# Optimization experiments

Hardware: AMD Instinct MI355X
Metric: run time of the kernel (lower is better)

## Reference

```python
import jax, jax.numpy as jnp
import numpy as np

BATCH = 8192
IN_FEATURES = 128
OUT_FEATURES = 256
GRID_SIZE = 20
ORDER = 3
L = GRID_SIZE + ORDER  # coeffs length per edge = 23


def setup_inputs() -> dict:
    key = jax.random.key(0)
    kx, kc = jax.random.split(key)
    x = jax.random.normal(kx, (BATCH, IN_FEATURES), dtype=jnp.float32)
    # fused per-edge B-spline coefficients: [out_features, in_features, grid_size+order]
    coeffs = jax.random.normal(kc, (OUT_FEATURES, IN_FEATURES, L), dtype=jnp.float32) * 0.1
    return {"x": x, "coeffs": coeffs}


def reference(x, coeffs):
    # x: [B, I], coeffs: [O, I, L]
    O, I, Lc = coeffs.shape
    B = x.shape[0]
    s = jax.nn.sigmoid(x)                      # x_clamped in (0, 1)
    idx = s * (GRID_SIZE - 1)                  # fractional bin index in [0, 19)
    k = idx.astype(jnp.int32)                  # trunc == floor since idx >= 0
    w1 = idx - k.astype(x.dtype)
    w0 = 1.0 - w1
    k0 = jnp.clip(k, 0, Lc - 1)                # [B, I]
    k1 = jnp.clip(k + 1, 0, Lc - 1)
    # Build sparse interpolation weights [B, I, L] (two nonzeros per (b, j)),
    # then contract against the shared coefficient tensor in one fused reduce:
    # out[b, i] = sum_j c[i, j, k0[b,j]] * w0[b,j] + c[i, j, k1[b,j]] * w1[b,j]
    brow = jnp.arange(B)[:, None]
    jcol = jnp.arange(I)[None, :]
    W = jnp.zeros((B, I, Lc), dtype=x.dtype)
    W = W.at[brow, jcol, k0].add(w0)
    W = W.at[brow, jcol, k1].add(w1)
    return jnp.einsum('bjl,ijl->bi', W, coeffs)  # [B, O]
```

## Files before the change

kernel.cpp:

```cpp
#include <hip/hip_runtime.h>
#include <hip/hip_fp16.h>

#define BATCH 8192
#define IN_F 128
#define OUT_F 256
#define LC 23
#define BROW 768
#define JPW 16

typedef _Float16 f16x8 __attribute__((ext_vector_type(8)));
typedef float f32x4 __attribute__((ext_vector_type(4)));
typedef _Float16 half2v __attribute__((ext_vector_type(2)));

__global__ __launch_bounds__(256) void prep_kernel(
    const float* __restrict__ coeffs, _Float16* __restrict__ cp2) {
    int t = blockIdx.x * 256 + threadIdx.x;
    int col = t & 15;
    int u = t >> 4;
    int q = u % 3;
    int v = u / 3;
    int g = v & 15;
    int j = v >> 4;
    int i = g * 16 + col;
    int s0 = q * 8;
    const float* src = coeffs + ((size_t)i * IN_F + j) * LC;
    f16x8 w;
#pragma unroll
    for (int e = 0; e < 8; ++e) {
        int s = s0 + e;
        float f = (s < 20) ? src[s] : 0.0f;
        w[e] = (_Float16)f;
    }
    char* dst = reinterpret_cast<char*>(cp2) +
                (size_t)(j * 16 + g) * BROW + q * 256 + col * 16;
    *reinterpret_cast<f16x8*>(dst) = w;
}

__global__ __launch_bounds__(512, 2) void kan_mfma7(
    const float* __restrict__ x, const char* __restrict__ cp2,
    float* __restrict__ out) {
    __shared__ uint2 mlds[IN_F][64];

    const int tid = threadIdx.x;
    const int lane = tid & 63;
    const int ks = tid >> 6;
    const int l15 = lane & 15;
    const int q = lane >> 4;
    const int q4 = q * 4;
    const int qc = (q < 3) ? q : 2;

    int wg = (blockIdx.x & 7) * 32 + (blockIdx.x >> 3);
    const int mb = wg >> 1;
    const int bn = wg & 1;
    const int b0 = mb * 64;

    {
        const int row = tid & 63;
        const int jb = (tid >> 6) * 16;
        const float4* xr = reinterpret_cast<const float4*>(
            x + (size_t)(b0 + row) * IN_F + jb);
#pragma unroll
        for (int u = 0; u < 4; ++u) {
            float4 xv = xr[u];
#pragma unroll
            for (int e = 0; e < 4; ++e) {
                float xvv = (e == 0) ? xv.x : (e == 1) ? xv.y
                           : (e == 2) ? xv.z : xv.w;
                float s = 1.0f / (1.0f + __expf(-xvv));
                float idxf = s * 19.0f;
                int k = (int)idxf;
                k = (k > 18) ? 18 : k;
                float w1 = idxf - (float)k;
                float w0 = 1.0f - w1;
                unsigned u0 = __half_as_ushort(__float2half(w0));
                unsigned u1 = __half_as_ushort(__float2half(w1));
                unsigned lo, hi;
                if (k & 1) { lo = u0 << 16; hi = u1; }
                else       { lo = u0 | (u1 << 16); hi = 0u; }
                unsigned P = (unsigned)(k >> 1);
                mlds[jb + u * 4 + e][row] = uint2{lo, hi | (P << 16)};
            }
        }
    }
    __syncthreads();

    const int j0 = ks * JPW;
    const char* bbase = cp2 + (size_t)(bn * 8) * BROW + qc * 256 + l15 * 16;
    auto bld = [&](int j, int nf) {
        return *reinterpret_cast<const f16x8*>(
            bbase + (size_t)(j * 16 + nf) * BROW);
    };

    f32x4 acc[4][8];
#pragma unroll
    for (int mf = 0; mf < 4; ++mf)
#pragma unroll
        for (int nf = 0; nf < 8; ++nf) acc[mf][nf] = f32x4{0.f, 0.f, 0.f, 0.f};

    f16x8 r1[4], r2[4];
#pragma unroll
    for (int h = 0; h < 4; ++h) r1[h] = bld(j0, h);

#pragma unroll 2
    for (int jj = 0; jj < JPW; ++jj) {
        const int j = j0 + jj;
#pragma unroll
        for (int h = 0; h < 4; ++h) r2[h] = bld(j, 4 + h);
        f16x8 au[4];
        {
            const uint2* mrow = &mlds[j][0];
#pragma unroll
            for (int mf = 0; mf < 4; ++mf) {
                uint2 m = mrow[mf * 16 + l15];
                unsigned lo = m.x;
                unsigned hi = m.y & 0xFFFFu;
                int d = (int)(m.y >> 16) - q4;
                union { uint32_t u[4]; f16x8 h; } a;
#pragma unroll
                for (int r = 0; r < 4; ++r) {
                    uint32_t v = (d == r) ? lo : 0u;
                    v = (d == r - 1) ? hi : v;
                    a.u[r] = v;
                }
                au[mf] = a.h;
            }
        }
#pragma unroll
        for (int mf = 0; mf < 4; ++mf)
#pragma unroll
            for (int nf = 0; nf < 4; ++nf)
                acc[mf][nf] = __builtin_amdgcn_mfma_f32_16x16x32_f16(
                    au[mf], r1[nf], acc[mf][nf], 0, 0, 0);
        if (jj + 1 < JPW) {
#pragma unroll
            for (int h = 0; h < 4; ++h) r1[h] = bld(j + 1, h);
        }
#pragma unroll
        for (int mf = 0; mf < 4; ++mf)
#pragma unroll
            for (int nf = 0; nf < 4; ++nf)
                acc[mf][4 + nf] = __builtin_amdgcn_mfma_f32_16x16x32_f16(
                    au[mf], r2[nf], acc[mf][4 + nf], 0, 0, 0);
    }

    __syncthreads();
    float* red = reinterpret_cast<float*>(&mlds[0][0]);
#pragma unroll
    for (int pass = 0; pass < 4; ++pass) {
#pragma unroll
        for (int mf = 0; mf < 4; ++mf)
#pragma unroll
            for (int t = 0; t < 2; ++t)
#pragma unroll
                for (int r = 0; r < 4; ++r)
                    red[ks * 2048 + (mf * 16 + q4 + r) * 32 + t * 16 + l15] =
                        acc[mf][pass * 2 + t][r];
        __syncthreads();
#pragma unroll
        for (int it = 0; it < 4; ++it) {
            int idx = it * 512 + tid;
            float s = 0.f;
#pragma unroll
            for (int w = 0; w < 8; ++w) s += red[w * 2048 + idx];
            int row = idx >> 5;
            int col = idx & 31;
            out[(size_t)(b0 + row) * OUT_F + bn * 128 + pass * 32 + col] = s;
        }
        __syncthreads();
    }
}

__device__ __forceinline__ float dot2_acc(unsigned cbits, unsigned wbits,
                                          float acc) {
#if __has_builtin(__builtin_amdgcn_fdot2)
    union { unsigned u; half2v h; } c, w;
    c.u = cbits; w.u = wbits;
    return __builtin_amdgcn_fdot2(c.h, w.h, acc, false);
#else
    __half2 hc = *reinterpret_cast<const __half2*>(&cbits);
    __half2 hw = *reinterpret_cast<const __half2*>(&wbits);
    float2 fc = __half22float2(hc);
    float2 fw = __half22float2(hw);
    return acc + fc.x * fw.x + fc.y * fw.y;
#endif
}

__global__ __launch_bounds__(256) void build_ctg_kernel(
    const float* __restrict__ coeffs, unsigned short* __restrict__ ctg) {
    int tid = blockIdx.x * 256 + threadIdx.x;
    int qq = tid & 63;
    int k = (tid >> 6) % LC;
    int j = tid / (64 * LC);
    if (j >= IN_F) return;
    int k1 = (k + 1 < LC) ? (k + 1) : (LC - 1);
    union { unsigned short h[8]; uint4 v; } u;
#pragma unroll
    for (int c = 0; c < 4; ++c) {
        int i = qq * 4 + c;
        const float* base = coeffs + ((size_t)i * IN_F + j) * LC;
        u.h[2 * c]     = __half_as_ushort(__float2half(base[k]));
        u.h[2 * c + 1] = __half_as_ushort(__float2half(base[k1]));
    }
    reinterpret_cast<uint4*>(ctg)[tid] = u.v;
}

__global__ __launch_bounds__(256) void kan_main_kernel(
    const float* __restrict__ x, const char* __restrict__ ctg,
    float* __restrict__ out) {
    __shared__ unsigned metas[4][2 * IN_F];
    const int wave = threadIdx.x >> 6;
    const int lane = threadIdx.x & 63;
    const int b = blockIdx.x * 4 + wave;
    float2 xv = reinterpret_cast<const float2*>(x + (size_t)b * IN_F)[lane];
    uint4 m;
#pragma unroll
    for (int t = 0; t < 2; ++t) {
        float xs = t ? xv.y : xv.x;
        float s = 1.0f / (1.0f + __expf(-xs));
        float idxf = s * 19.0f;
        int k = (int)idxf;
        k = (k > 18) ? 18 : k;
        float w1 = idxf - (float)k;
        float w0 = 1.0f - w1;
        int j = 2 * lane + t;
        unsigned off = (unsigned)((j * LC + k) << 10);
        half2v w; w[0] = (_Float16)w0; w[1] = (_Float16)w1;
        unsigned wbits = *reinterpret_cast<unsigned*>(&w);
        if (t == 0) { m.x = off; m.y = wbits; }
        else        { m.z = off; m.w = wbits; }
    }
    reinterpret_cast<uint4*>(&metas[wave][0])[lane] = m;
    __syncthreads();
    const unsigned lanebase = lane * 16;
    const uint4* mrow = reinterpret_cast<const uint4*>(&metas[wave][0]);
    float acc0 = 0.f, acc1 = 0.f, acc2 = 0.f, acc3 = 0.f;
#pragma unroll 8
    for (int j2 = 0; j2 < IN_F / 2; ++j2) {
        uint4 mm = mrow[j2];
        {
            const uint4 e = *reinterpret_cast<const uint4*>(
                ctg + (size_t)(lanebase + mm.x));
            acc0 = dot2_acc(e.x, mm.y, acc0);
            acc1 = dot2_acc(e.y, mm.y, acc1);
            acc2 = dot2_acc(e.z, mm.y, acc2);
            acc3 = dot2_acc(e.w, mm.y, acc3);
        }
        {
            const uint4 e = *reinterpret_cast<const uint4*>(
                ctg + (size_t)(lanebase + mm.z));
            acc0 = dot2_acc(e.x, mm.w, acc0);
            acc1 = dot2_acc(e.y, mm.w, acc1);
            acc2 = dot2_acc(e.z, mm.w, acc2);
            acc3 = dot2_acc(e.w, mm.w, acc3);
        }
    }
    float4 r = make_float4(acc0, acc1, acc2, acc3);
    reinterpret_cast<float4*>(out + (size_t)b * OUT_F)[lane] = r;
}

extern "C" void kernel_launch(void* const* d_in, const int* in_sizes, int n_in,
                              void* d_out, int out_size, void* d_ws,
                              size_t ws_size, hipStream_t stream) {
    const float* x = (const float*)d_in[0];
    const float* coeffs = (const float*)d_in[1];
    float* out = (float*)d_out;

    const size_t cp2_bytes = (size_t)IN_F * 16 * BROW;
    const size_t ctg_bytes = (size_t)IN_F * LC * 64 * 16;

    if (d_ws != nullptr && ws_size >= cp2_bytes) {
        _Float16* cp2 = (_Float16*)d_ws;
        prep_kernel<<<384, 256, 0, stream>>>(coeffs, cp2);
        kan_mfma7<<<256, 512, 0, stream>>>(x, (const char*)cp2, out);
    } else if (d_ws != nullptr && ws_size >= ctg_bytes) {
        char* ctg = (char*)d_ws;
        const int totalA = IN_F * LC * 64;
        build_ctg_kernel<<<(totalA + 255) / 256, 256, 0, stream>>>(
            coeffs, (unsigned short*)ctg);
        kan_main_kernel<<<BATCH / 4, 256, 0, stream>>>(x, ctg, out);
    } else {
        kan_main_kernel<<<BATCH / 4, 256, 0, stream>>>(x, (const char*)d_ws,
                                                       out);
    }
}
```

Baseline: 31.20 us.

## Halve output tile per block to double grid and raise occupancy

Each block now computes 64 output columns instead of 128, so the grid doubles to 512 blocks and launch bounds request 4 blocks per CU. The accumulator array and B-fragment registers halve, and the loop becomes a two-stage ping-pong prefetch of coefficient fragments. The reduction buffer writes use a swizzled column index to cut LDS bank conflicts, and one barrier is dropped. In exchange, the sigmoid/weight preprocessing of x is now repeated by twice as many blocks, and the LDS footprint (64 KB per block) may cap how many blocks actually reside per CU.

```diff
diff --git a/kernel.cpp b/kernel.cpp
--- a/kernel.cpp
+++ b/kernel.cpp
@@ -36,7 +36,7 @@
     *reinterpret_cast<f16x8*>(dst) = w;
 }
 
-__global__ __launch_bounds__(512, 2) void kan_mfma7(
+__global__ __launch_bounds__(512, 4) void kan_mfma8(
     const float* __restrict__ x, const char* __restrict__ cp2,
     float* __restrict__ out) {
     __shared__ uint2 mlds[IN_F][64];
@@ -49,14 +49,14 @@
     const int q4 = q * 4;
     const int qc = (q < 3) ? q : 2;
 
-    int wg = (blockIdx.x & 7) * 32 + (blockIdx.x >> 3);
-    const int mb = wg >> 1;
-    const int bn = wg & 1;
+    int wg = (blockIdx.x & 7) * 64 + (blockIdx.x >> 3);
+    const int mb = wg >> 2;
+    const int bn = wg & 3;
     const int b0 = mb * 64;
 
     {
-        const int row = tid & 63;
-        const int jb = (tid >> 6) * 16;
+        const int row = lane;
+        const int jb = ks * 16;
         const float4* xr = reinterpret_cast<const float4*>(
             x + (size_t)(b0 + row) * IN_F + jb);
 #pragma unroll
@@ -85,88 +85,77 @@
     __syncthreads();
 
     const int j0 = ks * JPW;
-    const char* bbase = cp2 + (size_t)(bn * 8) * BROW + qc * 256 + l15 * 16;
+    const char* bbase = cp2 + (size_t)(bn * 4) * BROW + qc * 256 + l15 * 16;
     auto bld = [&](int j, int nf) {
         return *reinterpret_cast<const f16x8*>(
             bbase + (size_t)(j * 16 + nf) * BROW);
     };
 
-    f32x4 acc[4][8];
+    f32x4 acc[4][4];
 #pragma unroll
     for (int mf = 0; mf < 4; ++mf)
 #pragma unroll
-        for (int nf = 0; nf < 8; ++nf) acc[mf][nf] = f32x4{0.f, 0.f, 0.f, 0.f};
-
-    f16x8 r1[4], r2[4];
-#pragma unroll
-    for (int h = 0; h < 4; ++h) r1[h] = bld(j0, h);
-
-#pragma unroll 2
-    for (int jj = 0; jj < JPW; ++jj) {
-        const int j = j0 + jj;
-#pragma unroll
-        for (int h = 0; h < 4; ++h) r2[h] = bld(j, 4 + h);
-        f16x8 au[4];
-        {
-            const uint2* mrow = &mlds[j][0];
-#pragma unroll
-            for (int mf = 0; mf < 4; ++mf) {
-                uint2 m = mrow[mf * 16 + l15];
-                unsigned lo = m.x;
-                unsigned hi = m.y & 0xFFFFu;
-                int d = (int)(m.y >> 16) - q4;
-                union { uint32_t u[4]; f16x8 h; } a;
-#pragma unroll
-                for (int r = 0; r < 4; ++r) {
-                    uint32_t v = (d == r) ? lo : 0u;
-                    v = (d == r - 1) ? hi : v;
-                    a.u[r] = v;
-                }
-                au[mf] = a.h;
+        for (int nf = 0; nf < 4; ++nf) acc[mf][nf] = f32x4{0.f, 0.f, 0.f, 0.f};
+
+    f16x8 rc[4], rn[4];
+#pragma unroll
+    for (int h = 0; h < 4; ++h) rc[h] = bld(j0, h);
+
+    auto step = [&](f16x8 (&cur)[4], f16x8 (&nxt)[4], int j, int jn) {
+#pragma unroll
+        for (int h = 0; h < 4; ++h) nxt[h] = bld(jn, h);
+#pragma unroll
+        for (int mf = 0; mf < 4; ++mf) {
+            uint2 m = mlds[j][mf * 16 + l15];
+            unsigned lo = m.x;
+            unsigned hi = m.y & 0xFFFFu;
+            int d = (int)(m.y >> 16) - q4;
+            union { uint32_t u[4]; f16x8 h; } au;
+#pragma unroll
+            for (int r = 0; r < 4; ++r) {
+                uint32_t v = (d == r) ? lo : 0u;
+                v = (d == r - 1) ? hi : v;
+                au.u[r] = v;
             }
-        }
-#pragma unroll
-        for (int mf = 0; mf < 4; ++mf)
 #pragma unroll
             for (int nf = 0; nf < 4; ++nf)
                 acc[mf][nf] = __builtin_amdgcn_mfma_f32_16x16x32_f16(
-                    au[mf], r1[nf], acc[mf][nf], 0, 0, 0);
-        if (jj + 1 < JPW) {
-#pragma unroll
-            for (int h = 0; h < 4; ++h) r1[h] = bld(j + 1, h);
-        }
-#pragma unroll
-        for (int mf = 0; mf < 4; ++mf)
-#pragma unroll
-            for (int nf = 0; nf < 4; ++nf)
-                acc[mf][4 + nf] = __builtin_amdgcn_mfma_f32_16x16x32_f16(
-                    au[mf], r2[nf], acc[mf][4 + nf], 0, 0, 0);
+                    au.h, cur[nf], acc[mf][nf], 0, 0, 0);
+        }
+    };
+
+    for (int jj = 0; jj < JPW; jj += 2) {
+        step(rc, rn, j0 + jj, j0 + jj + 1);
+        step(rn, rc, j0 + jj + 1, j0 + ((jj + 2) & (JPW - 1)));
     }
 
     __syncthreads();
     float* red = reinterpret_cast<float*>(&mlds[0][0]);
 #pragma unroll
-    for (int pass = 0; pass < 4; ++pass) {
+    for (int p = 0; p < 2; ++p) {
+        if (p) __syncthreads();
 #pragma unroll
         for (int mf = 0; mf < 4; ++mf)
 #pragma unroll
             for (int t = 0; t < 2; ++t)
 #pragma unroll
-                for (int r = 0; r < 4; ++r)
-                    red[ks * 2048 + (mf * 16 + q4 + r) * 32 + t * 16 + l15] =
-                        acc[mf][pass * 2 + t][r];
+                for (int r = 0; r < 4; ++r) {
+                    int colsw = (t * 16 + l15 + (q & 1) * 16) & 31;
+                    red[ks * 2048 + (mf * 16 + q4 + r) * 32 + colsw] =
+                        acc[mf][p * 2 + t][r];
+                }
         __syncthreads();
 #pragma unroll
         for (int it = 0; it < 4; ++it) {
             int idx = it * 512 + tid;
-            float s = 0.f;
-#pragma unroll
-            for (int w = 0; w < 8; ++w) s += red[w * 2048 + idx];
             int row = idx >> 5;
             int col = idx & 31;
-            out[(size_t)(b0 + row) * OUT_F + bn * 128 + pass * 32 + col] = s;
-        }
-        __syncthreads();
+            int colsw = (col + ((row >> 2) & 1) * 16) & 31;
+            float s = 0.f;
+#pragma unroll
+            for (int w = 0; w < 8; ++w) s += red[w * 2048 + row * 32 + colsw];
+            out[(size_t)(b0 + row) * OUT_F + bn * 64 + p * 32 + col] = s;
+        }
     }
 }
 
@@ -271,7 +260,7 @@
     if (d_ws != nullptr && ws_size >= cp2_bytes) {
         _Float16* cp2 = (_Float16*)d_ws;
         prep_kernel<<<384, 256, 0, stream>>>(coeffs, cp2);
-        kan_mfma7<<<256, 512, 0, stream>>>(x, (const char*)cp2, out);
+        kan_mfma8<<<512, 512, 0, stream>>>(x, (const char*)cp2, out);
     } else if (d_ws != nullptr && ws_size >= ctg_bytes) {
         char* ctg = (char*)d_ws;
         const int totalA = IN_F * LC * 64;
```

New measurement: 30.18 us. 3.3% less time.
